# Performance work log

Measured on AMD Instinct MI355X. Metric: run time of the kernel, lower is better.

## Reference

```python
import jax, jax.numpy as jnp
import numpy as np

# DeformConv1d config (matches init_kwargs)
K = 3          # kernel_size
DIL = 1        # dilation
STRIDE = 1
PAD = DIL * (K - 1)  # 'same' total padding = 2 -> (1,1) reflect


def setup_inputs() -> dict:
    key = jax.random.key(0)
    k1, k2, k3, k4 = jax.random.split(key, 4)
    B, C, L = 16, 64, 8192
    O = 64
    x = jax.random.normal(k1, (B, C, L), dtype=jnp.float32)
    offsets = jax.random.normal(k2, (B, 1, L, K), dtype=jnp.float32)
    weight = jax.random.normal(k3, (O, C, K), dtype=jnp.float32) * (1.0 / np.sqrt(C * K))
    bias = jax.random.normal(k4, (O,), dtype=jnp.float32) * 0.01
    return {"x": x, "offsets": offsets, "weight": weight, "bias": bias}


def _deform_conv1d(x, offsets, weight, bias):
    # reflect 'same' padding: left = PAD//2, right = PAD - PAD//2
    left = PAD // 2
    x_pad = jnp.pad(x, ((0, 0), (0, 0), (left, PAD - left)), mode="reflect")
    B, C, Lp = x_pad.shape
    OL = offsets.shape[-2]
    dt = x.dtype

    dilated = (jnp.arange(K, dtype=dt) * DIL)          # [K] = [0, d, ..., d(K-1)]
    t0 = (jnp.arange(OL, dtype=dt) * STRIDE)[:, None]  # [OL, 1]

    # sampling positions T: [B, G, OL, K], constrained to kernel receptive field
    T = t0 + dilated + offsets
    T = jnp.maximum(T, t0)
    T = jnp.minimum(T, t0 + dilated[-1])

    # integer lower neighbors (no grad through floor); clamp so U+1 is valid
    U = jnp.clip(jnp.floor(T).astype(jnp.int32), 0, Lp - 2)  # [B, G, OL, K]

    # gather both neighbors along length axis (broadcast offset group -> C)
    idx = jnp.broadcast_to(U, (B, C, OL, K)).reshape(B, C, OL * K)
    x0 = jnp.take_along_axis(x_pad, idx, axis=2).reshape(B, C, OL, K)
    x1 = jnp.take_along_axis(x_pad, idx + 1, axis=2).reshape(B, C, OL, K)

    # linear interpolation weights G = max(0, 1 - |U - T|)
    Uf = U.astype(dt)
    w0 = jnp.maximum(0.0, 1.0 - jnp.abs(Uf - T))        # [B, G, OL, K]
    w1 = jnp.maximum(0.0, 1.0 - jnp.abs(Uf + 1.0 - T))
    sampled = w0 * x0 + w1 * x1                          # [B, C, OL, K]

    # conv1d(weight, stride=K) on flattened [B, C, OL*K] == per-position contraction
    out = jnp.einsum("bcok,fck->bfo", sampled, weight) + bias[None, :, None]
    return out


def reference(x, offsets, weight, bias):
    return _deform_conv1d(x, offsets, weight, bias)
```

## Files before the change

### kernel.cpp

```cpp
#include <hip/hip_runtime.h>
#include <stdint.h>

#define BB   16
#define CC   64
#define LL   8192
#define OO   64
#define KK   3
#define TT   64
#define XSW  72

typedef __attribute__((ext_vector_type(8))) short short8;
typedef __attribute__((ext_vector_type(4))) float float4_t;

__device__ __forceinline__ ushort f2bf(float f) {
    uint32_t u = __float_as_uint(f);
    return (ushort)((u + 0x7FFFu + ((u >> 16) & 1u)) >> 16);
}
__device__ __forceinline__ float bf2f(ushort h) {
    return __uint_as_float(((uint32_t)h) << 16);
}

__global__ void wt_prep(const float* __restrict__ w, ushort* __restrict__ wt) {
    int idx = blockIdx.x * 256 + threadIdx.x;
    if (idx < OO * CC * KK) {
        int f = idx / (CC * KK);
        int rem = idx - f * (CC * KK);
        int c = rem / KK;
        int k = rem - c * KK;
        wt[f * (KK * CC) + k * CC + c] = f2bf(w[idx]);
    }
}

__global__ __launch_bounds__(256, 4) void deform_main(
    const float* __restrict__ x, const float* __restrict__ offs,
    const ushort* __restrict__ wt, const float* __restrict__ bias,
    float* __restrict__ out) {

    __shared__ ushort xs[67 * XSW];
    __shared__ int    Ul[TT * KK];
    __shared__ float  W0s[TT * KK], W1s[TT * KK];

    const int tid  = threadIdx.x;
    const int bb   = blockIdx.x >> 7;
    const int tile = blockIdx.x & 127;
    const int ts   = tile * TT;

    {
        const float* xb = x + (size_t)bb * (CC * LL);
        #pragma unroll
        for (int i = 0; i < 17; i++) {
            int idx = tid + i * 256;
            if (idx < 64 * 67) {
                int c = idx / 67;
                int p = idx - c * 67;
                int j = ts + p - 1;
                if (j < 0) j = -j;
                if (j >= LL) j = 2 * LL - 2 - j;
                xs[p * XSW + c] = f2bf(xb[c * LL + j]);
            }
        }
    }

    if (tid < TT * KK) {
        int n = tid / 3;
        int k = tid - n * 3;
        float off = offs[((size_t)bb * LL + ts + n) * 3 + k];
        float t0  = (float)(ts + n);
        float T   = t0 + (float)k + off;
        T = fmaxf(T, t0);
        T = fminf(T, t0 + 2.0f);
        int U = (int)floorf(T);
        if (U > LL) U = LL;
        float Uf = (float)U;
        Ul[tid]  = U - ts;
        W0s[tid] = fmaxf(0.0f, 1.0f - fabsf(Uf - T));
        W1s[tid] = fmaxf(0.0f, 1.0f - fabsf(Uf + 1.0f - T));
    }
    __syncthreads();

    const int lane = tid & 63;
    const int wv   = tid >> 6;
    const int lr   = lane & 15;
    const int q    = lane >> 4;
    const int n    = wv * 16 + lr;

    float4_t acc0 = {0.f, 0.f, 0.f, 0.f};
    float4_t acc1 = acc0, acc2 = acc0, acc3 = acc0;

    #pragma unroll
    for (int kk = 0; kk < 6; kk++) {
        const int k  = kk >> 1;
        const int k0 = kk * 32 + q * 8;
        const int c0 = k0 & 63;
        const int nk = n * KK + k;
        const int u  = Ul[nk];
        const float w0 = W0s[nk], w1 = W1s[nk];
        union { uint4 v; ushort u16[8]; } r0, r1;
        r0.v = *(const uint4*)&xs[u * XSW + c0];
        r1.v = *(const uint4*)&xs[(u + 1) * XSW + c0];
        union { short8 s; uint32_t u32[4]; } bf;
        #pragma unroll
        for (int j = 0; j < 4; j++) {
            float v0 = w0 * bf2f(r0.u16[2 * j])     + w1 * bf2f(r1.u16[2 * j]);
            float v1 = w0 * bf2f(r0.u16[2 * j + 1]) + w1 * bf2f(r1.u16[2 * j + 1]);
            bf.u32[j] = (uint32_t)f2bf(v0) | ((uint32_t)f2bf(v1) << 16);
        }
        short8 a0 = *(const short8*)&wt[(0 * 16 + lr) * (KK * CC) + k0];
        short8 a1 = *(const short8*)&wt[(1 * 16 + lr) * (KK * CC) + k0];
        short8 a2 = *(const short8*)&wt[(2 * 16 + lr) * (KK * CC) + k0];
        short8 a3 = *(const short8*)&wt[(3 * 16 + lr) * (KK * CC) + k0];
        acc0 = __builtin_amdgcn_mfma_f32_16x16x32_bf16(a0, bf.s, acc0, 0, 0, 0);
        acc1 = __builtin_amdgcn_mfma_f32_16x16x32_bf16(a1, bf.s, acc1, 0, 0, 0);
        acc2 = __builtin_amdgcn_mfma_f32_16x16x32_bf16(a2, bf.s, acc2, 0, 0, 0);
        acc3 = __builtin_amdgcn_mfma_f32_16x16x32_bf16(a3, bf.s, acc3, 0, 0, 0);
    }

    const int col = ts + wv * 16 + lr;
    float4_t accs[4] = {acc0, acc1, acc2, acc3};
    #pragma unroll
    for (int mt = 0; mt < 4; mt++) {
        const int f0 = mt * 16 + q * 4;
        float4_t bv = *(const float4_t*)&bias[f0];
        float* ob = out + ((size_t)bb * OO + f0) * LL + col;
        #pragma unroll
        for (int r = 0; r < 4; r++) {
            ob[(size_t)r * LL] = accs[mt][r] + bv[r];
        }
    }
}

extern "C" void kernel_launch(void* const* d_in, const int* in_sizes, int n_in,
                              void* d_out, int out_size, void* d_ws, size_t ws_size,
                              hipStream_t stream) {
    const float* x    = (const float*)d_in[0];
    const float* offs = (const float*)d_in[1];
    const float* w    = (const float*)d_in[2];
    const float* bias = (const float*)d_in[3];
    float* out = (float*)d_out;
    ushort* wt = (ushort*)d_ws;

    hipLaunchKernelGGL(wt_prep, dim3((OO * CC * KK + 255) / 256), dim3(256), 0, stream, w, wt);
    hipLaunchKernelGGL(deform_main, dim3(BB * (LL / TT)), dim3(256), 0, stream,
                       x, offs, wt, bias, out);
}
```

Baseline: 114.5 us.

## Stage x tile as fp32 via float4 loads and compute offsets in registers

The x tile is now staged in shared memory as fp32 using vectorized float4 global loads per channel row, replacing the scalar bf16-converting gather. Reflect padding is handled with special-case loads at the two edge tiles. Offset interpolation parameters are computed per thread in registers, which removes the shared-memory tables for U and the weights. The bf16 pack now uses the HIP intrinsic conversion. This doubles the LDS footprint per element and adds more LDS reads per MFMA step, but it cuts global load instructions and the per-element conversion work.

```diff
diff --git a/kernel.cpp b/kernel.cpp
--- a/kernel.cpp
+++ b/kernel.cpp
@@ -1,4 +1,5 @@
 #include <hip/hip_runtime.h>
+#include <hip/hip_bf16.h>
 #include <stdint.h>
 
 #define BB   16
@@ -7,7 +8,7 @@
 #define OO   64
 #define KK   3
 #define TT   64
-#define XSW  72
+#define XSW  68
 
 typedef __attribute__((ext_vector_type(8))) short short8;
 typedef __attribute__((ext_vector_type(4))) float float4_t;
@@ -16,8 +17,11 @@
     uint32_t u = __float_as_uint(f);
     return (ushort)((u + 0x7FFFu + ((u >> 16) & 1u)) >> 16);
 }
-__device__ __forceinline__ float bf2f(ushort h) {
-    return __uint_as_float(((uint32_t)h) << 16);
+
+__device__ __forceinline__ uint32_t pk2(float lo, float hi) {
+    float2 t; t.x = lo; t.y = hi;
+    __hip_bfloat162 h = __float22bfloat162_rn(t);
+    return *(uint32_t*)&h;
 }
 
 __global__ void wt_prep(const float* __restrict__ w, ushort* __restrict__ wt) {
@@ -36,75 +40,77 @@
     const ushort* __restrict__ wt, const float* __restrict__ bias,
     float* __restrict__ out) {
 
-    __shared__ ushort xs[67 * XSW];
-    __shared__ int    Ul[TT * KK];
-    __shared__ float  W0s[TT * KK], W1s[TT * KK];
+    __shared__ float xs[72 * XSW];
 
     const int tid  = threadIdx.x;
     const int bb   = blockIdx.x >> 7;
     const int tile = blockIdx.x & 127;
     const int ts   = tile * TT;
+    const int lane = tid & 63;
+    const int wv   = tid >> 6;
 
     {
         const float* xb = x + (size_t)bb * (CC * LL);
+        const int c     = wv * 16 + (lane >> 2);
+        const int fb    = lane & 3;
+        const float* xrow = xb + (size_t)c * LL;
         #pragma unroll
-        for (int i = 0; i < 17; i++) {
-            int idx = tid + i * 256;
-            if (idx < 64 * 67) {
-                int c = idx / 67;
-                int p = idx - c * 67;
-                int j = ts + p - 1;
-                if (j < 0) j = -j;
-                if (j >= LL) j = 2 * LL - 2 - j;
-                xs[p * XSW + c] = f2bf(xb[c * LL + j]);
+        for (int i = 0; i < 5; i++) {
+            int fi = fb + 4 * i;
+            int j0 = ts - 4 + 4 * fi;
+            if (fi < 18 && j0 >= 0 && j0 <= LL - 4) {
+                float4 v = *(const float4*)(xrow + j0);
+                float* dst = &xs[(4 * fi) * XSW + c];
+                dst[0 * XSW] = v.x; dst[1 * XSW] = v.y;
+                dst[2 * XSW] = v.z; dst[3 * XSW] = v.w;
             }
         }
+        if (tile == 0   && tid < 64) xs[3 * XSW + tid]  = xb[(size_t)tid * LL + 1];
+        if (tile == 127 && tid < 64) xs[68 * XSW + tid] = xb[(size_t)tid * LL + (LL - 2)];
     }
 
-    if (tid < TT * KK) {
-        int n = tid / 3;
-        int k = tid - n * 3;
-        float off = offs[((size_t)bb * LL + ts + n) * 3 + k];
-        float t0  = (float)(ts + n);
-        float T   = t0 + (float)k + off;
-        T = fmaxf(T, t0);
-        T = fminf(T, t0 + 2.0f);
-        int U = (int)floorf(T);
-        if (U > LL) U = LL;
-        float Uf = (float)U;
-        Ul[tid]  = U - ts;
-        W0s[tid] = fmaxf(0.0f, 1.0f - fabsf(Uf - T));
-        W1s[tid] = fmaxf(0.0f, 1.0f - fabsf(Uf + 1.0f - T));
+    const int lr = lane & 15;
+    const int q  = lane >> 4;
+    const int n  = wv * 16 + lr;
+    int   ppk[KK];
+    float w0k[KK], w1k[KK];
+    {
+        const float* ob = offs + ((size_t)bb * LL + ts + n) * KK;
+        const float t0 = (float)(ts + n);
+        #pragma unroll
+        for (int k = 0; k < KK; k++) {
+            float T = t0 + (float)k + ob[k];
+            T = fmaxf(T, t0);
+            T = fminf(T, t0 + 2.0f);
+            int U = (int)floorf(T);
+            if (U > LL) U = LL;
+            float Uf = (float)U;
+            ppk[k] = U - ts + 3;
+            w0k[k] = fmaxf(0.0f, 1.0f - fabsf(Uf - T));
+            w1k[k] = fmaxf(0.0f, 1.0f - fabsf(Uf + 1.0f - T));
+        }
     }
     __syncthreads();
-
-    const int lane = tid & 63;
-    const int wv   = tid >> 6;
-    const int lr   = lane & 15;
-    const int q    = lane >> 4;
-    const int n    = wv * 16 + lr;
 
     float4_t acc0 = {0.f, 0.f, 0.f, 0.f};
     float4_t acc1 = acc0, acc2 = acc0, acc3 = acc0;
 
     #pragma unroll
     for (int kk = 0; kk < 6; kk++) {
-        const int k  = kk >> 1;
         const int k0 = kk * 32 + q * 8;
+        const int k  = k0 >> 6;
         const int c0 = k0 & 63;
-        const int nk = n * KK + k;
-        const int u  = Ul[nk];
-        const float w0 = W0s[nk], w1 = W1s[nk];
-        union { uint4 v; ushort u16[8]; } r0, r1;
-        r0.v = *(const uint4*)&xs[u * XSW + c0];
-        r1.v = *(const uint4*)&xs[(u + 1) * XSW + c0];
+        const int pp = ppk[k];
+        const float w0 = w0k[k], w1 = w1k[k];
+        const float4 r0a = *(const float4*)&xs[pp * XSW + c0];
+        const float4 r0b = *(const float4*)&xs[pp * XSW + c0 + 4];
+        const float4 r1a = *(const float4*)&xs[(pp + 1) * XSW + c0];
+        const float4 r1b = *(const float4*)&xs[(pp + 1) * XSW + c0 + 4];
         union { short8 s; uint32_t u32[4]; } bf;
-        #pragma unroll
-        for (int j = 0; j < 4; j++) {
-            float v0 = w0 * bf2f(r0.u16[2 * j])     + w1 * bf2f(r1.u16[2 * j]);
-            float v1 = w0 * bf2f(r0.u16[2 * j + 1]) + w1 * bf2f(r1.u16[2 * j + 1]);
-            bf.u32[j] = (uint32_t)f2bf(v0) | ((uint32_t)f2bf(v1) << 16);
-        }
+        bf.u32[0] = pk2(w0 * r0a.x + w1 * r1a.x, w0 * r0a.y + w1 * r1a.y);
+        bf.u32[1] = pk2(w0 * r0a.z + w1 * r1a.z, w0 * r0a.w + w1 * r1a.w);
+        bf.u32[2] = pk2(w0 * r0b.x + w1 * r1b.x, w0 * r0b.y + w1 * r1b.y);
+        bf.u32[3] = pk2(w0 * r0b.z + w1 * r1b.z, w0 * r0b.w + w1 * r1b.w);
         short8 a0 = *(const short8*)&wt[(0 * 16 + lr) * (KK * CC) + k0];
         short8 a1 = *(const short8*)&wt[(1 * 16 + lr) * (KK * CC) + k0];
         short8 a2 = *(const short8*)&wt[(2 * 16 + lr) * (KK * CC) + k0];
```

Result: no change. 113.4 us (-1.0%).
